# Kernel optimization log

Measured on AMD Instinct MI355X. Metric: run time of the kernel, lower is better.

Reference implementation:

```python
import jax, jax.numpy as jnp
import numpy as np

N1 = 100000  # source cloud size (x1)
N2 = 100000  # target cloud size (x2)
F = 64       # point feature dim
E = 1600000  # number of radius edges (avg 16 neighbors)
H = 128      # MLP hidden/out dim


def setup_inputs() -> dict:
    key = jax.random.key(0)
    ks = jax.random.split(key, 12)
    s = 0.05
    return {
        "x1_features": jax.random.normal(ks[0], (N1, F), jnp.float32),
        "x1_pos": jax.random.normal(ks[1], (N1, 3), jnp.float32),
        "x2_features": jax.random.normal(ks[2], (N2, F), jnp.float32),
        "x2_pos": jax.random.normal(ks[3], (N2, 3), jnp.float32),
        "W1": jax.random.normal(ks[4], (2 * F + 3, H), jnp.float32) * s,
        "b1": jnp.zeros((H,), jnp.float32),
        "W2": jax.random.normal(ks[5], (H, H), jnp.float32) * s,
        "b2": jnp.zeros((H,), jnp.float32),
        "W3": jax.random.normal(ks[6], (H, H), jnp.float32) * s,
        "b3": jnp.zeros((H,), jnp.float32),
        "edge_src": jax.random.randint(ks[7], (E,), 0, N1, jnp.int32),
        "edge_dst": jax.random.randint(ks[8], (E,), 0, N2, jnp.int32),
    }


def reference(x1_features, x1_pos, x2_features, x2_pos,
              W1, b1, W2, b2, W3, b3, edge_src, edge_dst):
    # message(x_i, x_j, pos_i, pos_j): i = target (x2, edge_dst), j = source (x1, edge_src)
    # msg = cat([x_i, x_j, pos_j - pos_i], dim=1)  -> [E, 2F+3]
    msg = jnp.concatenate(
        [x2_features[edge_dst],
         x1_features[edge_src],
         x1_pos[edge_src] - x2_pos[edge_dst]], axis=1)
    # MLP (Linear+ReLU x3, FastFlow3D make_mlp style)
    h = jax.nn.relu(msg @ W1 + b1)
    h = jax.nn.relu(h @ W2 + b2)
    h = jax.nn.relu(h @ W3 + b3)
    # scatter-max aggregation onto x2 nodes; PyG fills empty segments with 0
    out = jax.ops.segment_max(h, edge_dst, num_segments=N2)
    out = jnp.where(jnp.isneginf(out), 0.0, out)
    return out, x2_pos
```

## Files before the change

kernel.cpp:

```cpp
#include <hip/hip_runtime.h>
#include <hip/hip_bf16.h>

#define DEV __device__ __forceinline__

typedef short bf16x8 __attribute__((ext_vector_type(8)));
typedef float f32x16 __attribute__((ext_vector_type(16)));

static constexpr int FDIM  = 64;
static constexpr int HH    = 128;
static constexpr int K1RAW = 2 * FDIM + 3;
static constexpr int K1    = 160;
static constexpr int KS1   = K1 / 16;
static constexpr int KS2   = HH / 16;
static constexpr int TM    = 128;

static constexpr int MSTR  = 2 * K1;
static constexpr int HSTR  = 2 * HH;
static constexpr int L_MSG = 0;
static constexpr int L_H   = TM * MSTR;
static constexpr int L_DST = L_H + TM * HSTR;
static constexpr int L_TOT = L_DST + TM * 4;

static constexpr int WT1_ELEMS = HH * K1;
static constexpr int WT2_ELEMS = HH * HH;
static constexpr int WT_TOTAL  = WT1_ELEMS + 2 * WT2_ELEMS;

DEV unsigned pack2(float a, float b) {
    union { __hip_bfloat162 h; unsigned u; } cv;
    cv.h.x = __float2bfloat16(a);
    cv.h.y = __float2bfloat16(b);
    return cv.u;
}
DEV unsigned short f2bf(float f) {
    union { __hip_bfloat16 h; unsigned short u; } cv;
    cv.h = __float2bfloat16(f);
    return cv.u;
}
DEV int swz_msg(int c, int r) { const int m = (c < 16) ? 7 : 3; return (c & ~m) | ((c ^ r) & m); }
DEV int swz_h(int c, int r)   { return (c & ~7) | ((c ^ r) & 7); }

__global__ void k_cvt(const float* __restrict__ src, unsigned short* __restrict__ dst, int n8) {
    int i = blockIdx.x * 256 + threadIdx.x;
    if (i < n8) {
        float4 a = *(const float4*)(src + (size_t)i * 8);
        float4 b = *(const float4*)(src + (size_t)i * 8 + 4);
        uint4 o;
        o.x = pack2(a.x, a.y); o.y = pack2(a.z, a.w);
        o.z = pack2(b.x, b.y); o.w = pack2(b.z, b.w);
        *(uint4*)(dst + (size_t)i * 8) = o;
    }
}

__global__ void k_wprep(const float* __restrict__ W1, const float* __restrict__ W2,
                        const float* __restrict__ W3, unsigned short* __restrict__ wt) {
    int i = blockIdx.x * 256 + threadIdx.x;
    if (i < WT1_ELEMS) {
        int n = i / K1, k = i % K1;
        float v = (k < K1RAW) ? W1[k * HH + n] : 0.f;
        wt[i] = f2bf(v);
    } else if (i < WT1_ELEMS + WT2_ELEMS) {
        int j = i - WT1_ELEMS; int n = j / HH, k = j % HH;
        wt[i] = f2bf(W2[k * HH + n]);
    } else if (i < WT_TOTAL) {
        int j = i - WT1_ELEMS - WT2_ELEMS; int n = j / HH, k = j % HH;
        wt[i] = f2bf(W3[k * HH + n]);
    }
}

__global__ void k_hist(const int* __restrict__ edst, int* __restrict__ cnt, int E) {
    int e = blockIdx.x * 256 + threadIdx.x;
    if (e < E) atomicAdd(&cnt[edst[e]], 1);
}

__global__ void k_scan_part(const int* __restrict__ cnt, int* __restrict__ partial, int n2) {
    __shared__ int sm[256];
    int t = threadIdx.x;
    int base = blockIdx.x * 1024 + t * 4;
    int s = 0;
#pragma unroll
    for (int j = 0; j < 4; j++) { int idx = base + j; if (idx < n2) s += cnt[idx]; }
    sm[t] = s; __syncthreads();
    for (int off = 128; off > 0; off >>= 1) {
        if (t < off) sm[t] += sm[t + off];
        __syncthreads();
    }
    if (t == 0) partial[blockIdx.x] = sm[0];
}

__global__ void k_scan_top(int* __restrict__ partial, int nb) {
    __shared__ int sm[256];
    int t = threadIdx.x;
    int v = (t < nb) ? partial[t] : 0;
    sm[t] = v; __syncthreads();
    for (int off = 1; off < 256; off <<= 1) {
        int add = (t >= off) ? sm[t - off] : 0;
        __syncthreads();
        sm[t] += add;
        __syncthreads();
    }
    if (t < nb) partial[t] = sm[t] - v;
}

__global__ void k_scan_down(const int* __restrict__ cnt, const int* __restrict__ partial,
                            int* __restrict__ cursor, int n2) {
    __shared__ int sm[256];
    int t = threadIdx.x;
    int base = blockIdx.x * 1024 + t * 4;
    int c[4]; int s = 0;
#pragma unroll
    for (int j = 0; j < 4; j++) { int idx = base + j; c[j] = (idx < n2) ? cnt[idx] : 0; s += c[j]; }
    sm[t] = s; __syncthreads();
    for (int off = 1; off < 256; off <<= 1) {
        int add = (t >= off) ? sm[t - off] : 0;
        __syncthreads();
        sm[t] += add;
        __syncthreads();
    }
    int run = partial[blockIdx.x] + (sm[t] - s);
#pragma unroll
    for (int j = 0; j < 4; j++) {
        int idx = base + j;
        if (idx < n2) cursor[idx] = run;
        run += c[j];
    }
}

__global__ void k_fill(const int* __restrict__ edst, int* __restrict__ cursor,
                       int* __restrict__ csr_e, int* __restrict__ csr_d, int E) {
    int e = blockIdx.x * 256 + threadIdx.x;
    if (e < E) {
        int d = edst[e];
        int p = atomicAdd(&cursor[d], 1);
        csr_e[p] = e;
        csr_d[p] = d;
    }
}

DEV f32x16 zerov() {
    f32x16 v;
#pragma unroll
    for (int i = 0; i < 16; i++) v[i] = 0.f;
    return v;
}

template <int KSTEPS, int STRIDE, bool MSG>
DEV void layer_mfma(const unsigned short* __restrict__ wtl, const char* __restrict__ src,
                    int rt, int ct0, int l31, int hh, f32x16 acc[2]) {
#pragma unroll
    for (int ks = 0; ks < KSTEPS; ks++) {
        const int kk = ks * 16 + 8 * hh;
        bf16x8 A = *(const bf16x8*)(wtl + (rt * 32 + l31) * (KSTEPS * 16) + kk);
        const int c  = 2 * ks + hh;
        const int cs = MSG ? swz_msg(c, l31) : swz_h(c, l31);
        bf16x8 B0 = *(const bf16x8*)(src + ((ct0)     * 32 + l31) * STRIDE + cs * 16);
        bf16x8 B1 = *(const bf16x8*)(src + ((ct0 + 1) * 32 + l31) * STRIDE + cs * 16);
        acc[0] = __builtin_amdgcn_mfma_f32_32x32x16_bf16(A, B0, acc[0], 0, 0, 0);
        acc[1] = __builtin_amdgcn_mfma_f32_32x32x16_bf16(A, B1, acc[1], 0, 0, 0);
    }
}

template <int STRIDE>
DEV void layer_store(f32x16 acc[2], const float* __restrict__ bias, char* __restrict__ hb,
                     int rt, int ct0, int l31, int hh) {
#pragma unroll
    for (int j = 0; j < 2; j++) {
        const int r = (ct0 + j) * 32 + l31;
#pragma unroll
        for (int g = 0; g < 4; g++) {
            float4 bv = *(const float4*)(bias + rt * 32 + 8 * g + 4 * hh);
            float v0 = fmaxf(acc[j][4 * g + 0] + bv.x, 0.f);
            float v1 = fmaxf(acc[j][4 * g + 1] + bv.y, 0.f);
            float v2 = fmaxf(acc[j][4 * g + 2] + bv.z, 0.f);
            float v3 = fmaxf(acc[j][4 * g + 3] + bv.w, 0.f);
            uint2 w; w.x = pack2(v0, v1); w.y = pack2(v2, v3);
            *(uint2*)(hb + r * STRIDE + swz_h(4 * rt + g, r) * 16 + 8 * hh) = w;
        }
    }
}

template <bool SORTED, bool BF16SRC>
__global__ __launch_bounds__(512, 4) void k_main(
    const float* __restrict__ x1f, const float* __restrict__ x1p,
    const float* __restrict__ x2f, const float* __restrict__ x2p,
    const char* __restrict__ xb1, const char* __restrict__ xb2,
    const float* __restrict__ b1, const float* __restrict__ b2, const float* __restrict__ b3,
    const unsigned short* __restrict__ wt,
    const int* __restrict__ csr_e, const int* __restrict__ csr_d,
    const int* __restrict__ edge_src, const int* __restrict__ edge_dst,
    float* __restrict__ out, int E) {
    __shared__ __align__(16) char sm[L_TOT];
    char* msg = sm + L_MSG;
    char* hbf = sm + L_H;
    int*  dl  = (int*)(sm + L_DST);

    const int tid  = threadIdx.x;
    const int lane = tid & 63;
    const int wv   = tid >> 6;
    const int l31  = lane & 31;
    const int hh   = lane >> 5;
    const int eb   = blockIdx.x * TM;

    {
        const int r   = tid >> 2;
        const int sub = tid & 3;
        const int slot = eb + r;
        const bool ok = slot < E;
        int e = 0, d = 0, s = 0;
        if (ok) {
            if (SORTED) { e = csr_e[slot]; d = csr_d[slot]; }
            else        { e = slot;        d = edge_dst[e]; }
            s = edge_src[e];
        }
        if (sub == 0) dl[r] = ok ? d : -1;
        char* row = msg + r * MSTR;
        const int c0 = sub * 4;
#pragma unroll
        for (int i = 0; i < 4; i++) {
            const int c = c0 + i;
            uint4 v; v.x = v.y = v.z = v.w = 0u;
            if (ok) {
                if (BF16SRC) {
                    const char* base = (sub < 2) ? (xb2 + (size_t)d * (2 * FDIM))
                                                 : (xb1 + (size_t)s * (2 * FDIM));
                    const int cc = (sub < 2) ? c : (c - 8);
                    v = *(const uint4*)(base + cc * 16);
                } else {
                    const float* base = (sub < 2) ? (x2f + (size_t)d * FDIM)
                                                  : (x1f + (size_t)s * FDIM);
                    const int cc = (sub < 2) ? c : (c - 8);
                    float4 a = *(const float4*)(base + cc * 8);
                    float4 b = *(const float4*)(base + cc * 8 + 4);
                    v.x = pack2(a.x, a.y); v.y = pack2(a.z, a.w);
                    v.z = pack2(b.x, b.y); v.w = pack2(b.z, b.w);
                }
            }
            *(uint4*)(row + swz_msg(c, r) * 16) = v;
        }
        if (sub == 3) {
            float dx = 0.f, dy = 0.f, dz = 0.f;
            if (ok) {
                dx = x1p[s * 3 + 0] - x2p[d * 3 + 0];
                dy = x1p[s * 3 + 1] - x2p[d * 3 + 1];
                dz = x1p[s * 3 + 2] - x2p[d * 3 + 2];
            }
            uint2 w; w.x = pack2(dx, dy); w.y = pack2(dz, 0.f);
            *(uint2*)(row + swz_msg(16, r) * 16 + 0) = w;
            uint2 z2; z2.x = 0u; z2.y = 0u;
            *(uint2*)(row + swz_msg(16, r) * 16 + 8) = z2;
            uint4 z4; z4.x = z4.y = z4.z = z4.w = 0u;
            *(uint4*)(row + swz_msg(17, r) * 16) = z4;
            *(uint4*)(row + swz_msg(18, r) * 16) = z4;
            *(uint4*)(row + swz_msg(19, r) * 16) = z4;
        }
    }
    __syncthreads();

    const int rt  = wv & 3;
    const int ct0 = (wv >> 2) * 2;
    f32x16 acc[2];

    acc[0] = zerov(); acc[1] = zerov();
    layer_mfma<KS1, MSTR, true>(wt, msg, rt, ct0, l31, hh, acc);
    layer_store<HSTR>(acc, b1, hbf, rt, ct0, l31, hh);
    __syncthreads();

    acc[0] = zerov(); acc[1] = zerov();
    layer_mfma<KS2, HSTR, false>(wt + WT1_ELEMS, hbf, rt, ct0, l31, hh, acc);
    layer_store<MSTR>(acc, b2, msg, rt, ct0, l31, hh);
    __syncthreads();

    acc[0] = zerov(); acc[1] = zerov();
    layer_mfma<KS2, MSTR, false>(wt + WT1_ELEMS + WT2_ELEMS, msg, rt, ct0, l31, hh, acc);
    layer_store<HSTR>(acc, b3, hbf, rt, ct0, l31, hh);
    __syncthreads();

    {
        const int cpair = tid & 63;
        const int strip = tid >> 6;
        const int r0 = strip * 16;
        int curd = dl[r0];
        float m0 = 0.f, m1 = 0.f;
        for (int r = r0; r < r0 + 16; r++) {
            int d = dl[r];
            if (d != curd) {
                if (curd >= 0) {
                    if (m0 > 0.f) atomicMax((int*)out + (size_t)curd * HH + 2 * cpair,     __float_as_int(m0));
                    if (m1 > 0.f) atomicMax((int*)out + (size_t)curd * HH + 2 * cpair + 1, __float_as_int(m1));
                }
                curd = d; m0 = 0.f; m1 = 0.f;
            }
            unsigned w = *(const unsigned*)(hbf + r * HSTR + swz_h(cpair >> 2, r) * 16 + (cpair & 3) * 4);
            m0 = fmaxf(m0, __uint_as_float(w << 16));
            m1 = fmaxf(m1, __uint_as_float(w & 0xffff0000u));
        }
        if (curd >= 0) {
            if (m0 > 0.f) atomicMax((int*)out + (size_t)curd * HH + 2 * cpair,     __float_as_int(m0));
            if (m1 > 0.f) atomicMax((int*)out + (size_t)curd * HH + 2 * cpair + 1, __float_as_int(m1));
        }
    }
}

extern "C" void kernel_launch(void* const* d_in, const int* in_sizes, int n_in,
                              void* d_out, int out_size, void* d_ws, size_t ws_size,
                              hipStream_t stream) {
    const float* x1f = (const float*)d_in[0];
    const float* x1p = (const float*)d_in[1];
    const float* x2f = (const float*)d_in[2];
    const float* x2p = (const float*)d_in[3];
    const float* W1  = (const float*)d_in[4];
    const float* b1  = (const float*)d_in[5];
    const float* W2  = (const float*)d_in[6];
    const float* b2  = (const float*)d_in[7];
    const float* W3  = (const float*)d_in[8];
    const float* b3  = (const float*)d_in[9];
    const int* esrc  = (const int*)d_in[10];
    const int* edst  = (const int*)d_in[11];
    const int E  = in_sizes[10];
    const int N1 = in_sizes[1] / 3;
    const int N2 = in_sizes[3] / 3;
    float* out = (float*)d_out;

    size_t off = 0;
    auto take = [&](size_t bytes) { size_t o = off; off = (off + bytes + 255) & ~(size_t)255; return o; };
    size_t o_cnt = take(4 * (size_t)N2);
    size_t o_cur = take(4 * (size_t)N2);
    size_t o_par = take(4 * 256);
    size_t o_ce  = take(4 * (size_t)E);
    size_t o_cd  = take(4 * (size_t)E);
    size_t o_wt  = take(2 * (size_t)WT_TOTAL);
    size_t need_csr = off;
    size_t o_x1  = take(2 * (size_t)N1 * FDIM);
    size_t o_x2  = take(2 * (size_t)N2 * FDIM);
    size_t need_bf = off;

    const int NB = (N2 + 1023) / 1024;
    bool use_csr = (need_csr <= ws_size) && (NB <= 256);
    bool use_bf  = (need_bf <= ws_size);

    char* ws = (char*)d_ws;
    unsigned short* wt = use_csr ? (unsigned short*)(ws + o_wt) : (unsigned short*)ws;
    int* cnt    = (int*)(ws + o_cnt);
    int* cursor = (int*)(ws + o_cur);
    int* part   = (int*)(ws + o_par);
    int* csr_e  = (int*)(ws + o_ce);
    int* csr_d  = (int*)(ws + o_cd);
    char* xb1   = ws + o_x1;
    char* xb2   = ws + o_x2;

    (void)hipMemsetAsync(out, 0, (size_t)N2 * HH * 4, stream);
    (void)hipMemcpyAsync(out + (size_t)N2 * HH, x2p, (size_t)N2 * 3 * 4,
                         hipMemcpyDeviceToDevice, stream);

    k_wprep<<<(WT_TOTAL + 255) / 256, 256, 0, stream>>>(W1, W2, W3, wt);

    if (use_bf) {
        int n8_1 = N1 * FDIM / 8, n8_2 = N2 * FDIM / 8;
        k_cvt<<<(n8_1 + 255) / 256, 256, 0, stream>>>(x1f, (unsigned short*)xb1, n8_1);
        k_cvt<<<(n8_2 + 255) / 256, 256, 0, stream>>>(x2f, (unsigned short*)xb2, n8_2);
    }

    const int grid = (E + TM - 1) / TM;
    if (use_csr) {
        (void)hipMemsetAsync(cnt, 0, 4 * (size_t)N2, stream);
        k_hist<<<(E + 255) / 256, 256, 0, stream>>>(edst, cnt, E);
        k_scan_part<<<NB, 256, 0, stream>>>(cnt, part, N2);
        k_scan_top<<<1, 256, 0, stream>>>(part, NB);
        k_scan_down<<<NB, 256, 0, stream>>>(cnt, part, cursor, N2);
        k_fill<<<(E + 255) / 256, 256, 0, stream>>>(edst, cursor, csr_e, csr_d, E);
        if (use_bf)
            k_main<true, true><<<grid, 512, 0, stream>>>(
                x1f, x1p, x2f, x2p, xb1, xb2, b1, b2, b3, wt, csr_e, csr_d, esrc, edst, out, E);
        else
            k_main<true, false><<<grid, 512, 0, stream>>>(
                x1f, x1p, x2f, x2p, xb1, xb2, b1, b2, b3, wt, csr_e, csr_d, esrc, edst, out, E);
    } else {
        if (use_bf)
            k_main<false, true><<<grid, 512, 0, stream>>>(
                x1f, x1p, x2f, x2p, xb1, xb2, b1, b2, b3, wt, edst, edst, esrc, edst, out, E);
        else
            k_main<false, false><<<grid, 512, 0, stream>>>(
                x1f, x1p, x2f, x2p, xb1, xb2, b1, b2, b3, wt, edst, edst, esrc, edst, out, E);
    }
}
```

Baseline: 605.8 us.

## Keep MLP hidden activations in registers across layers, cutting LDS round-trips

Each wave now owns 32 edge rows and computes all 128 output columns, so layers 2 and 3 take their B operand from the previous layer's packed bf16 accumulators via lane shuffles instead of LDS. This drops the separate hidden LDS buffer and the barriers between layers. It also trims K1 padding from 160 to 144 and moves to 256-thread blocks. The cost is a much larger register footprint (four accumulators plus 32 packed words), and every wave now reads the full weight matrix rather than a quarter of it.

```diff
diff --git a/kernel.cpp b/kernel.cpp
--- a/kernel.cpp
+++ b/kernel.cpp
@@ -9,17 +9,12 @@
 static constexpr int FDIM  = 64;
 static constexpr int HH    = 128;
 static constexpr int K1RAW = 2 * FDIM + 3;
-static constexpr int K1    = 160;
+static constexpr int K1    = 144;
 static constexpr int KS1   = K1 / 16;
-static constexpr int KS2   = HH / 16;
 static constexpr int TM    = 128;
 
 static constexpr int MSTR  = 2 * K1;
-static constexpr int HSTR  = 2 * HH;
-static constexpr int L_MSG = 0;
-static constexpr int L_H   = TM * MSTR;
-static constexpr int L_DST = L_H + TM * HSTR;
-static constexpr int L_TOT = L_DST + TM * 4;
+static constexpr int L_TOT = TM * MSTR + TM * 4;
 
 static constexpr int WT1_ELEMS = HH * K1;
 static constexpr int WT2_ELEMS = HH * HH;
@@ -36,8 +31,7 @@
     cv.h = __float2bfloat16(f);
     return cv.u;
 }
-DEV int swz_msg(int c, int r) { const int m = (c < 16) ? 7 : 3; return (c & ~m) | ((c ^ r) & m); }
-DEV int swz_h(int c, int r)   { return (c & ~7) | ((c ^ r) & 7); }
+DEV int swz_msg(int c, int r) { const int m = (c < 16) ? 7 : 1; return (c & ~m) | ((c ^ r) & m); }
 
 __global__ void k_cvt(const float* __restrict__ src, unsigned short* __restrict__ dst, int n8) {
     int i = blockIdx.x * 256 + threadIdx.x;
@@ -143,43 +137,44 @@
     return v;
 }
 
-template <int KSTEPS, int STRIDE, bool MSG>
-DEV void layer_mfma(const unsigned short* __restrict__ wtl, const char* __restrict__ src,
-                    int rt, int ct0, int l31, int hh, f32x16 acc[2]) {
-#pragma unroll
-    for (int ks = 0; ks < KSTEPS; ks++) {
-        const int kk = ks * 16 + 8 * hh;
-        bf16x8 A = *(const bf16x8*)(wtl + (rt * 32 + l31) * (KSTEPS * 16) + kk);
-        const int c  = 2 * ks + hh;
-        const int cs = MSG ? swz_msg(c, l31) : swz_h(c, l31);
-        bf16x8 B0 = *(const bf16x8*)(src + ((ct0)     * 32 + l31) * STRIDE + cs * 16);
-        bf16x8 B1 = *(const bf16x8*)(src + ((ct0 + 1) * 32 + l31) * STRIDE + cs * 16);
-        acc[0] = __builtin_amdgcn_mfma_f32_32x32x16_bf16(A, B0, acc[0], 0, 0, 0);
-        acc[1] = __builtin_amdgcn_mfma_f32_32x32x16_bf16(A, B1, acc[1], 0, 0, 0);
-    }
-}
-
-template <int STRIDE>
-DEV void layer_store(f32x16 acc[2], const float* __restrict__ bias, char* __restrict__ hb,
-                     int rt, int ct0, int l31, int hh) {
-#pragma unroll
-    for (int j = 0; j < 2; j++) {
-        const int r = (ct0 + j) * 32 + l31;
-#pragma unroll
-        for (int g = 0; g < 4; g++) {
-            float4 bv = *(const float4*)(bias + rt * 32 + 8 * g + 4 * hh);
-            float v0 = fmaxf(acc[j][4 * g + 0] + bv.x, 0.f);
-            float v1 = fmaxf(acc[j][4 * g + 1] + bv.y, 0.f);
-            float v2 = fmaxf(acc[j][4 * g + 2] + bv.z, 0.f);
-            float v3 = fmaxf(acc[j][4 * g + 3] + bv.w, 0.f);
-            uint2 w; w.x = pack2(v0, v1); w.y = pack2(v2, v3);
-            *(uint2*)(hb + r * STRIDE + swz_h(4 * rt + g, r) * 16 + 8 * hh) = w;
+DEV void pk_prep(const f32x16 a[4], const float* __restrict__ bias, int hh, unsigned pk[32]) {
+#pragma unroll
+    for (int u = 0; u < 16; u++) {
+        const int t = u >> 2, g = u & 3;
+        float4 bv = *(const float4*)(bias + 8 * u + 4 * hh);
+        float v0 = fmaxf(a[t][4 * g + 0] + bv.x, 0.f);
+        float v1 = fmaxf(a[t][4 * g + 1] + bv.y, 0.f);
+        float v2 = fmaxf(a[t][4 * g + 2] + bv.z, 0.f);
+        float v3 = fmaxf(a[t][4 * g + 3] + bv.w, 0.f);
+        pk[2 * u + 0] = pack2(v0, v1);
+        pk[2 * u + 1] = pack2(v2, v3);
+    }
+}
+
+DEV void layer_reg(const unsigned short* __restrict__ wtl, const unsigned pk[32],
+                   int l31, int hh, f32x16 c[4]) {
+#pragma unroll
+    for (int ks = 0; ks < 8; ks++) {
+        const int u0 = 2 * ks, u1 = 2 * ks + 1;
+        int s0 = __shfl_xor((int)pk[2 * u1 + 0], 32, 64);
+        int s1 = __shfl_xor((int)pk[2 * u1 + 1], 32, 64);
+        int s2 = __shfl_xor((int)pk[2 * u0 + 0], 32, 64);
+        int s3 = __shfl_xor((int)pk[2 * u0 + 1], 32, 64);
+        union { unsigned u[4]; bf16x8 v; } B;
+        B.u[0] = (hh == 0) ? pk[2 * u0 + 0] : (unsigned)s0;
+        B.u[1] = (hh == 0) ? pk[2 * u0 + 1] : (unsigned)s1;
+        B.u[2] = (hh == 0) ? (unsigned)s2 : pk[2 * u1 + 0];
+        B.u[3] = (hh == 0) ? (unsigned)s3 : pk[2 * u1 + 1];
+#pragma unroll
+        for (int t = 0; t < 4; t++) {
+            bf16x8 A = *(const bf16x8*)(wtl + (t * 32 + l31) * HH + ks * 16 + 8 * hh);
+            c[t] = __builtin_amdgcn_mfma_f32_32x32x16_bf16(A, B.v, c[t], 0, 0, 0);
         }
     }
 }
 
 template <bool SORTED, bool BF16SRC>
-__global__ __launch_bounds__(512, 4) void k_main(
+__global__ __launch_bounds__(256, 3) void k_main(
     const float* __restrict__ x1f, const float* __restrict__ x1p,
     const float* __restrict__ x2f, const float* __restrict__ x2p,
     const char* __restrict__ xb1, const char* __restrict__ xb2,
@@ -189,9 +184,8 @@
     const int* __restrict__ edge_src, const int* __restrict__ edge_dst,
     float* __restrict__ out, int E) {
     __shared__ __align__(16) char sm[L_TOT];
-    char* msg = sm + L_MSG;
-    char* hbf = sm + L_H;
-    int*  dl  = (int*)(sm + L_DST);
+    char* msg = sm;
+    int*  dl  = (int*)(sm + TM * MSTR);
 
     const int tid  = threadIdx.x;
     const int lane = tid & 63;
@@ -201,8 +195,8 @@
     const int eb   = blockIdx.x * TM;
 
     {
-        const int r   = tid >> 2;
-        const int sub = tid & 3;
+        const int r   = tid >> 1;
+        const int sub = tid & 1;
         const int slot = eb + r;
         const bool ok = slot < E;
         int e = 0, d = 0, s = 0;
@@ -213,74 +207,86 @@
         }
         if (sub == 0) dl[r] = ok ? d : -1;
         char* row = msg + r * MSTR;
-        const int c0 = sub * 4;
-#pragma unroll
-        for (int i = 0; i < 4; i++) {
+        const int c0 = sub * 8;
+#pragma unroll
+        for (int i = 0; i < 8; i++) {
             const int c = c0 + i;
             uint4 v; v.x = v.y = v.z = v.w = 0u;
             if (ok) {
                 if (BF16SRC) {
-                    const char* base = (sub < 2) ? (xb2 + (size_t)d * (2 * FDIM))
-                                                 : (xb1 + (size_t)s * (2 * FDIM));
-                    const int cc = (sub < 2) ? c : (c - 8);
-                    v = *(const uint4*)(base + cc * 16);
+                    const char* base = (sub == 0) ? (xb2 + (size_t)d * (2 * FDIM))
+                                                  : (xb1 + (size_t)s * (2 * FDIM));
+                    v = *(const uint4*)(base + i * 16);
                 } else {
-                    const float* base = (sub < 2) ? (x2f + (size_t)d * FDIM)
-                                                  : (x1f + (size_t)s * FDIM);
-                    const int cc = (sub < 2) ? c : (c - 8);
-                    float4 a = *(const float4*)(base + cc * 8);
-                    float4 b = *(const float4*)(base + cc * 8 + 4);
+                    const float* base = (sub == 0) ? (x2f + (size_t)d * FDIM)
+                                                   : (x1f + (size_t)s * FDIM);
+                    float4 a = *(const float4*)(base + i * 8);
+                    float4 b = *(const float4*)(base + i * 8 + 4);
                     v.x = pack2(a.x, a.y); v.y = pack2(a.z, a.w);
                     v.z = pack2(b.x, b.y); v.w = pack2(b.z, b.w);
                 }
             }
             *(uint4*)(row + swz_msg(c, r) * 16) = v;
         }
-        if (sub == 3) {
+        if (sub == 1) {
             float dx = 0.f, dy = 0.f, dz = 0.f;
             if (ok) {
                 dx = x1p[s * 3 + 0] - x2p[d * 3 + 0];
                 dy = x1p[s * 3 + 1] - x2p[d * 3 + 1];
                 dz = x1p[s * 3 + 2] - x2p[d * 3 + 2];
             }
-            uint2 w; w.x = pack2(dx, dy); w.y = pack2(dz, 0.f);
-            *(uint2*)(row + swz_msg(16, r) * 16 + 0) = w;
-            uint2 z2; z2.x = 0u; z2.y = 0u;
-            *(uint2*)(row + swz_msg(16, r) * 16 + 8) = z2;
-            uint4 z4; z4.x = z4.y = z4.z = z4.w = 0u;
-            *(uint4*)(row + swz_msg(17, r) * 16) = z4;
-            *(uint4*)(row + swz_msg(18, r) * 16) = z4;
-            *(uint4*)(row + swz_msg(19, r) * 16) = z4;
+            uint4 v; v.x = pack2(dx, dy); v.y = pack2(dz, 0.f); v.z = 0u; v.w = 0u;
+            *(uint4*)(row + swz_msg(16, r) * 16) = v;
+            uint4 z; z.x = z.y = z.z = z.w = 0u;
+            *(uint4*)(row + swz_msg(17, r) * 16) = z;
         }
     }
     __syncthreads();
 
-    const int rt  = wv & 3;
-    const int ct0 = (wv >> 2) * 2;
-    f32x16 acc[2];
-
-    acc[0] = zerov(); acc[1] = zerov();
-    layer_mfma<KS1, MSTR, true>(wt, msg, rt, ct0, l31, hh, acc);
-    layer_store<HSTR>(acc, b1, hbf, rt, ct0, l31, hh);
-    __syncthreads();
-
-    acc[0] = zerov(); acc[1] = zerov();
-    layer_mfma<KS2, HSTR, false>(wt + WT1_ELEMS, hbf, rt, ct0, l31, hh, acc);
-    layer_store<MSTR>(acc, b2, msg, rt, ct0, l31, hh);
-    __syncthreads();
-
-    acc[0] = zerov(); acc[1] = zerov();
-    layer_mfma<KS2, MSTR, false>(wt + WT1_ELEMS + WT2_ELEMS, msg, rt, ct0, l31, hh, acc);
-    layer_store<HSTR>(acc, b3, hbf, rt, ct0, l31, hh);
+    const int myrow = wv * 32 + l31;
+    const char* mrow = msg + myrow * MSTR;
+
+    f32x16 a[4];
+    a[0] = zerov(); a[1] = zerov(); a[2] = zerov(); a[3] = zerov();
+#pragma unroll
+    for (int ks = 0; ks < KS1; ks++) {
+        bf16x8 B = *(const bf16x8*)(mrow + swz_msg(2 * ks + hh, myrow) * 16);
+#pragma unroll
+        for (int t = 0; t < 4; t++) {
+            bf16x8 A = *(const bf16x8*)(wt + (t * 32 + l31) * K1 + ks * 16 + 8 * hh);
+            a[t] = __builtin_amdgcn_mfma_f32_32x32x16_bf16(A, B, a[t], 0, 0, 0);
+        }
+    }
+
+    unsigned pk[32];
+    pk_prep(a, b1, hh, pk);
+
+    f32x16 c[4];
+    c[0] = zerov(); c[1] = zerov(); c[2] = zerov(); c[3] = zerov();
+    layer_reg(wt + WT1_ELEMS, pk, l31, hh, c);
+    pk_prep(c, b2, hh, pk);
+
+    a[0] = zerov(); a[1] = zerov(); a[2] = zerov(); a[3] = zerov();
+    layer_reg(wt + WT1_ELEMS + WT2_ELEMS, pk, l31, hh, a);
+    pk_prep(a, b3, hh, pk);
+
+    {
+        char* hrow = msg + myrow * MSTR;
+#pragma unroll
+        for (int u = 0; u < 16; u++) {
+            uint2 w; w.x = pk[2 * u + 0]; w.y = pk[2 * u + 1];
+            *(uint2*)(hrow + swz_msg(u, myrow) * 16 + 8 * hh) = w;
+        }
+    }
     __syncthreads();
 
     {
         const int cpair = tid & 63;
         const int strip = tid >> 6;
-        const int r0 = strip * 16;
+        const int r0 = strip * 32;
         int curd = dl[r0];
         float m0 = 0.f, m1 = 0.f;
-        for (int r = r0; r < r0 + 16; r++) {
+        for (int r = r0; r < r0 + 32; r++) {
             int d = dl[r];
             if (d != curd) {
                 if (curd >= 0) {
@@ -289,7 +295,7 @@
                 }
                 curd = d; m0 = 0.f; m1 = 0.f;
             }
-            unsigned w = *(const unsigned*)(hbf + r * HSTR + swz_h(cpair >> 2, r) * 16 + (cpair & 3) * 4);
+            unsigned w = *(const unsigned*)(msg + r * MSTR + swz_msg(cpair >> 2, r) * 16 + (cpair & 3) * 4);
             m0 = fmaxf(m0, __uint_as_float(w << 16));
             m1 = fmaxf(m1, __uint_as_float(w & 0xffff0000u));
         }
@@ -368,17 +374,17 @@
         k_scan_down<<<NB, 256, 0, stream>>>(cnt, part, cursor, N2);
         k_fill<<<(E + 255) / 256, 256, 0, stream>>>(edst, cursor, csr_e, csr_d, E);
         if (use_bf)
-            k_main<true, true><<<grid, 512, 0, stream>>>(
+            k_main<true, true><<<grid, 256, 0, stream>>>(
                 x1f, x1p, x2f, x2p, xb1, xb2, b1, b2, b3, wt, csr_e, csr_d, esrc, edst, out, E);
         else
-            k_main<true, false><<<grid, 512, 0, stream>>>(
+            k_main<true, false><<<grid, 256, 0, stream>>>(
                 x1f, x1p, x2f, x2p, xb1, xb2, b1, b2, b3, wt, csr_e, csr_d, esrc, edst, out, E);
     } else {
         if (use_bf)
-            k_main<false, true><<<grid, 512, 0, stream>>>(
+            k_main<false, true><<<grid, 256, 0, stream>>>(
                 x1f, x1p, x2f, x2p, xb1, xb2, b1, b2, b3, wt, edst, edst, esrc, edst, out, E);
         else
-            k_main<false, false><<<grid, 512, 0, stream>>>(
+            k_main<false, false><<<grid, 256, 0, stream>>>(
                 x1f, x1p, x2f, x2p, xb1, xb2, b1, b2, b3, wt, edst, edst, esrc, edst, out, E);
     }
 }
```

After: 908.1 us. 49.9% more time.

## Halve edge tile to 64 rows, trim K padding, double occupancy

Applied to the files above, without the earlier changes.

Shrinks the per-block edge tile from 128 to 64 rows so each wave computes a single 32x32 output tile per layer, and raises launch bounds to 8 blocks per CU. Layer-1 K padding drops from 160 to 144, with the swizzle mask adjusted for the shorter rows. The gather and segment-max phases are remapped to the new thread-to-row layout, with one feature per thread in the reduction. The aim is lower LDS and register use per block for more concurrent blocks and latency hiding, plus less padded MFMA work. The cost is twice as many blocks, more atomics at tile boundaries, and less weight reuse per block.

```diff
diff --git a/kernel.cpp b/kernel.cpp
--- a/kernel.cpp
+++ b/kernel.cpp
@@ -9,10 +9,10 @@
 static constexpr int FDIM  = 64;
 static constexpr int HH    = 128;
 static constexpr int K1RAW = 2 * FDIM + 3;
-static constexpr int K1    = 160;
+static constexpr int K1    = 144;
 static constexpr int KS1   = K1 / 16;
 static constexpr int KS2   = HH / 16;
-static constexpr int TM    = 128;
+static constexpr int TM    = 64;
 
 static constexpr int MSTR  = 2 * K1;
 static constexpr int HSTR  = 2 * HH;
@@ -36,7 +36,7 @@
     cv.h = __float2bfloat16(f);
     return cv.u;
 }
-DEV int swz_msg(int c, int r) { const int m = (c < 16) ? 7 : 3; return (c & ~m) | ((c ^ r) & m); }
+DEV int swz_msg(int c, int r) { const int m = (c < 16) ? 7 : 1; return (c & ~m) | ((c ^ r) & m); }
 DEV int swz_h(int c, int r)   { return (c & ~7) | ((c ^ r) & 7); }
 
 __global__ void k_cvt(const float* __restrict__ src, unsigned short* __restrict__ dst, int n8) {
@@ -143,43 +143,38 @@
     return v;
 }
 
-template <int KSTEPS, int STRIDE, bool MSG>
-DEV void layer_mfma(const unsigned short* __restrict__ wtl, const char* __restrict__ src,
-                    int rt, int ct0, int l31, int hh, f32x16 acc[2]) {
-#pragma unroll
-    for (int ks = 0; ks < KSTEPS; ks++) {
-        const int kk = ks * 16 + 8 * hh;
-        bf16x8 A = *(const bf16x8*)(wtl + (rt * 32 + l31) * (KSTEPS * 16) + kk);
-        const int c  = 2 * ks + hh;
-        const int cs = MSG ? swz_msg(c, l31) : swz_h(c, l31);
-        bf16x8 B0 = *(const bf16x8*)(src + ((ct0)     * 32 + l31) * STRIDE + cs * 16);
-        bf16x8 B1 = *(const bf16x8*)(src + ((ct0 + 1) * 32 + l31) * STRIDE + cs * 16);
-        acc[0] = __builtin_amdgcn_mfma_f32_32x32x16_bf16(A, B0, acc[0], 0, 0, 0);
-        acc[1] = __builtin_amdgcn_mfma_f32_32x32x16_bf16(A, B1, acc[1], 0, 0, 0);
-    }
-}
-
 template <int STRIDE>
-DEV void layer_store(f32x16 acc[2], const float* __restrict__ bias, char* __restrict__ hb,
-                     int rt, int ct0, int l31, int hh) {
-#pragma unroll
-    for (int j = 0; j < 2; j++) {
-        const int r = (ct0 + j) * 32 + l31;
-#pragma unroll
-        for (int g = 0; g < 4; g++) {
-            float4 bv = *(const float4*)(bias + rt * 32 + 8 * g + 4 * hh);
-            float v0 = fmaxf(acc[j][4 * g + 0] + bv.x, 0.f);
-            float v1 = fmaxf(acc[j][4 * g + 1] + bv.y, 0.f);
-            float v2 = fmaxf(acc[j][4 * g + 2] + bv.z, 0.f);
-            float v3 = fmaxf(acc[j][4 * g + 3] + bv.w, 0.f);
-            uint2 w; w.x = pack2(v0, v1); w.y = pack2(v2, v3);
-            *(uint2*)(hb + r * STRIDE + swz_h(4 * rt + g, r) * 16 + 8 * hh) = w;
-        }
-    }
+DEV void tile_store(f32x16 acc, const float* __restrict__ bias, char* __restrict__ hb,
+                    int rt, int ct, int l31, int hh) {
+    const int r = ct * 32 + l31;
+#pragma unroll
+    for (int g = 0; g < 4; g++) {
+        float4 bv = *(const float4*)(bias + rt * 32 + 8 * g + 4 * hh);
+        float v0 = fmaxf(acc[4 * g + 0] + bv.x, 0.f);
+        float v1 = fmaxf(acc[4 * g + 1] + bv.y, 0.f);
+        float v2 = fmaxf(acc[4 * g + 2] + bv.z, 0.f);
+        float v3 = fmaxf(acc[4 * g + 3] + bv.w, 0.f);
+        uint2 w; w.x = pack2(v0, v1); w.y = pack2(v2, v3);
+        *(uint2*)(hb + r * STRIDE + swz_h(4 * rt + g, r) * 16 + 8 * hh) = w;
+    }
+}
+
+template <int STRIDE>
+DEV f32x16 layer128(const unsigned short* __restrict__ wtl, const char* __restrict__ src,
+                    int rt, int ct, int l31, int hh) {
+    f32x16 acc = zerov();
+#pragma unroll
+    for (int ks = 0; ks < KS2; ks++) {
+        bf16x8 A = *(const bf16x8*)(wtl + (rt * 32 + l31) * HH + ks * 16 + 8 * hh);
+        const int r = ct * 32 + l31;
+        bf16x8 B = *(const bf16x8*)(src + r * STRIDE + swz_h(2 * ks + hh, r) * 16);
+        acc = __builtin_amdgcn_mfma_f32_32x32x16_bf16(A, B, acc, 0, 0, 0);
+    }
+    return acc;
 }
 
 template <bool SORTED, bool BF16SRC>
-__global__ __launch_bounds__(512, 4) void k_main(
+__global__ __launch_bounds__(512, 8) void k_main(
     const float* __restrict__ x1f, const float* __restrict__ x1p,
     const float* __restrict__ x2f, const float* __restrict__ x2p,
     const char* __restrict__ xb1, const char* __restrict__ xb2,
@@ -201,8 +196,8 @@
     const int eb   = blockIdx.x * TM;
 
     {
-        const int r   = tid >> 2;
-        const int sub = tid & 3;
+        const int r   = tid >> 3;
+        const int sub = tid & 7;
         const int slot = eb + r;
         const bool ok = slot < E;
         int e = 0, d = 0, s = 0;
@@ -211,23 +206,20 @@
             else        { e = slot;        d = edge_dst[e]; }
             s = edge_src[e];
         }
-        if (sub == 0) dl[r] = ok ? d : -1;
         char* row = msg + r * MSTR;
-        const int c0 = sub * 4;
-#pragma unroll
-        for (int i = 0; i < 4; i++) {
-            const int c = c0 + i;
+#pragma unroll
+        for (int i = 0; i < 2; i++) {
+            const int c = 2 * sub + i;
             uint4 v; v.x = v.y = v.z = v.w = 0u;
             if (ok) {
+                const int cc = c & 7;
                 if (BF16SRC) {
-                    const char* base = (sub < 2) ? (xb2 + (size_t)d * (2 * FDIM))
-                                                 : (xb1 + (size_t)s * (2 * FDIM));
-                    const int cc = (sub < 2) ? c : (c - 8);
+                    const char* base = (c < 8) ? (xb2 + (size_t)d * (2 * FDIM))
+                                               : (xb1 + (size_t)s * (2 * FDIM));
                     v = *(const uint4*)(base + cc * 16);
                 } else {
-                    const float* base = (sub < 2) ? (x2f + (size_t)d * FDIM)
-                                                  : (x1f + (size_t)s * FDIM);
-                    const int cc = (sub < 2) ? c : (c - 8);
+                    const float* base = (c < 8) ? (x2f + (size_t)d * FDIM)
+                                                : (x1f + (size_t)s * FDIM);
                     float4 a = *(const float4*)(base + cc * 8);
                     float4 b = *(const float4*)(base + cc * 8 + 4);
                     v.x = pack2(a.x, a.y); v.y = pack2(a.z, a.w);
@@ -236,67 +228,69 @@
             }
             *(uint4*)(row + swz_msg(c, r) * 16) = v;
         }
-        if (sub == 3) {
+        if (sub == 0) {
+            dl[r] = ok ? d : -1;
             float dx = 0.f, dy = 0.f, dz = 0.f;
             if (ok) {
                 dx = x1p[s * 3 + 0] - x2p[d * 3 + 0];
                 dy = x1p[s * 3 + 1] - x2p[d * 3 + 1];
                 dz = x1p[s * 3 + 2] - x2p[d * 3 + 2];
             }
-            uint2 w; w.x = pack2(dx, dy); w.y = pack2(dz, 0.f);
-            *(uint2*)(row + swz_msg(16, r) * 16 + 0) = w;
-            uint2 z2; z2.x = 0u; z2.y = 0u;
-            *(uint2*)(row + swz_msg(16, r) * 16 + 8) = z2;
-            uint4 z4; z4.x = z4.y = z4.z = z4.w = 0u;
-            *(uint4*)(row + swz_msg(17, r) * 16) = z4;
-            *(uint4*)(row + swz_msg(18, r) * 16) = z4;
-            *(uint4*)(row + swz_msg(19, r) * 16) = z4;
+            uint4 v; v.x = pack2(dx, dy); v.y = pack2(dz, 0.f); v.z = 0u; v.w = 0u;
+            *(uint4*)(row + swz_msg(16, r) * 16) = v;
+        } else if (sub == 1) {
+            uint4 z; z.x = z.y = z.z = z.w = 0u;
+            *(uint4*)(row + swz_msg(17, r) * 16) = z;
         }
     }
     __syncthreads();
 
-    const int rt  = wv & 3;
-    const int ct0 = (wv >> 2) * 2;
-    f32x16 acc[2];
-
-    acc[0] = zerov(); acc[1] = zerov();
-    layer_mfma<KS1, MSTR, true>(wt, msg, rt, ct0, l31, hh, acc);
-    layer_store<HSTR>(acc, b1, hbf, rt, ct0, l31, hh);
+    const int rt = wv & 3;
+    const int ct = wv >> 2;
+
+    {
+        f32x16 acc = zerov();
+#pragma unroll
+        for (int ks = 0; ks < KS1; ks++) {
+            bf16x8 A = *(const bf16x8*)(wt + (rt * 32 + l31) * K1 + ks * 16 + 8 * hh);
+            const int r = ct * 32 + l31;
+            bf16x8 B = *(const bf16x8*)(msg + r * MSTR + swz_msg(2 * ks + hh, r) * 16);
+            acc = __builtin_amdgcn_mfma_f32_32x32x16_bf16(A, B, acc, 0, 0, 0);
+        }
+        tile_store<HSTR>(acc, b1, hbf, rt, ct, l31, hh);
+    }
     __syncthreads();
 
-    acc[0] = zerov(); acc[1] = zerov();
-    layer_mfma<KS2, HSTR, false>(wt + WT1_ELEMS, hbf, rt, ct0, l31, hh, acc);
-    layer_store<MSTR>(acc, b2, msg, rt, ct0, l31, hh);
+    {
+        f32x16 acc = layer128<HSTR>(wt + WT1_ELEMS, hbf, rt, ct, l31, hh);
+        tile_store<MSTR>(acc, b2, msg, rt, ct, l31, hh);
+    }
     __syncthreads();
 
-    acc[0] = zerov(); acc[1] = zerov();
-    layer_mfma<KS2, MSTR, false>(wt + WT1_ELEMS + WT2_ELEMS, msg, rt, ct0, l31, hh, acc);
-    layer_store<HSTR>(acc, b3, hbf, rt, ct0, l31, hh);
+    {
+        f32x16 acc = layer128<MSTR>(wt + WT1_ELEMS + WT2_ELEMS, msg, rt, ct, l31, hh);
+        tile_store<HSTR>(acc, b3, hbf, rt, ct, l31, hh);
+    }
     __syncthreads();
 
     {
-        const int cpair = tid & 63;
-        const int strip = tid >> 6;
+        const int feat  = tid & 127;
+        const int strip = tid >> 7;
         const int r0 = strip * 16;
         int curd = dl[r0];
-        float m0 = 0.f, m1 = 0.f;
+        float m = 0.f;
         for (int r = r0; r < r0 + 16; r++) {
             int d = dl[r];
             if (d != curd) {
-                if (curd >= 0) {
-                    if (m0 > 0.f) atomicMax((int*)out + (size_t)curd * HH + 2 * cpair,     __float_as_int(m0));
-                    if (m1 > 0.f) atomicMax((int*)out + (size_t)curd * HH + 2 * cpair + 1, __float_as_int(m1));
-                }
-                curd = d; m0 = 0.f; m1 = 0.f;
+                if (curd >= 0 && m > 0.f)
+                    atomicMax((int*)out + (size_t)curd * HH + feat, __float_as_int(m));
+                curd = d; m = 0.f;
             }
-            unsigned w = *(const unsigned*)(hbf + r * HSTR + swz_h(cpair >> 2, r) * 16 + (cpair & 3) * 4);
-            m0 = fmaxf(m0, __uint_as_float(w << 16));
-            m1 = fmaxf(m1, __uint_as_float(w & 0xffff0000u));
-        }
-        if (curd >= 0) {
-            if (m0 > 0.f) atomicMax((int*)out + (size_t)curd * HH + 2 * cpair,     __float_as_int(m0));
-            if (m1 > 0.f) atomicMax((int*)out + (size_t)curd * HH + 2 * cpair + 1, __float_as_int(m1));
-        }
+            unsigned short w = *(const unsigned short*)(hbf + r * HSTR + swz_h(feat >> 3, r) * 16 + (feat & 7) * 2);
+            m = fmaxf(m, __uint_as_float(((unsigned)w) << 16));
+        }
+        if (curd >= 0 && m > 0.f)
+            atomicMax((int*)out + (size_t)curd * HH + feat, __float_as_int(m));
     }
 }
 
```

After: 824.6 us. +36.1%, slower.
